# Performance work log

Measured on AMD Instinct MI355X. Metric: run time of the kernel, lower is better.

Reference implementation:

```python
import jax, jax.numpy as jnp
import numpy as np

N_NODES = 50000
N_EDGES = 800000
D_IN = 64
D_OUT = 64


def setup_inputs() -> dict:
    key = jax.random.key(0)
    k_feat, k_src, k_dst, k_ew, k_wn, k_bn, k_ws = jax.random.split(key, 7)
    feat = jax.random.normal(k_feat, (N_NODES, D_IN), dtype=jnp.float32)
    src = jax.random.randint(k_src, (N_EDGES,), 0, N_NODES, dtype=jnp.int64)
    dst = jax.random.randint(k_dst, (N_EDGES,), 0, N_NODES, dtype=jnp.int64)
    edge_weight = jax.random.uniform(k_ew, (N_EDGES,), dtype=jnp.float32)
    W_neigh = jax.random.normal(k_wn, (D_IN, D_OUT), dtype=jnp.float32) / np.sqrt(D_IN)
    b_neigh = jax.random.normal(k_bn, (D_OUT,), dtype=jnp.float32) * 0.01
    W_self = jax.random.normal(k_ws, (D_OUT, D_IN), dtype=jnp.float32) / np.sqrt(D_IN)
    return {"feat": feat, "src": src, "dst": dst, "edge_weight": edge_weight,
            "W_neigh": W_neigh, "b_neigh": b_neigh, "W_self": W_self}


def reference(feat, src, dst, edge_weight, W_neigh, b_neigh, W_self):
    # DGL GraphConv with norm='none': sum_{j in N(i)} e_ij * h_j, then @ W + b
    msg = feat[src] * edge_weight[:, None]                      # [E, D_in]
    agg = jax.ops.segment_sum(msg, dst, num_segments=feat.shape[0])  # [N, D_in]
    neigh_feat = agg @ W_neigh + b_neigh                        # [N, D_out]
    self_feat = feat @ W_self.T                                 # Linear, bias=False
    return neigh_feat + self_feat
```

## Files before the change

### kernel.cpp

```cpp
#include <hip/hip_runtime.h>

#define NN 50000
#define NE 800000
#define D 64
#define BN_SH 8
#define BNODES 256
#define NB 196
#define EPB 4096
#define NWB 196
#define CONV_B 800
#define BCAP 4608

constexpr size_t alignup(size_t x) { return (x + 1023) & ~size_t(1023); }
constexpr size_t OFF_EM   = 0;
constexpr size_t OFF_EM2  = alignup(OFF_EM + (size_t)NB * BCAP * 8);
constexpr size_t OFF_AGG  = alignup(OFF_EM2 + (size_t)NB * BCAP * 4);
constexpr size_t OFF_FB   = alignup(OFF_AGG + (size_t)NN * D * 4);
constexpr size_t OFF_RS2  = alignup(OFF_FB + (size_t)NN * D * 2);
constexpr size_t OFF_CUR  = alignup(OFF_RS2 + (size_t)NN * 8);

__device__ __forceinline__ unsigned f2bf(unsigned u) {
    return (u + 0x7FFFu + ((u >> 16) & 1u)) >> 16;
}

__global__ __launch_bounds__(256) void gc_zero(int* cur) {
    if (threadIdx.x < NB) cur[threadIdx.x] = 0;
}

__global__ __launch_bounds__(256) void bin_write(const int* __restrict__ src,
                                                 const int* __restrict__ dst,
                                                 const float* __restrict__ ew,
                                                 const float* __restrict__ feat,
                                                 int* __restrict__ cur,
                                                 uint2* __restrict__ em,
                                                 ushort* __restrict__ fb16) {
    int b = blockIdx.x;
    if (b >= NWB) {
        int cb = b - NWB;
        const float4* f4 = (const float4*)feat;
        ushort4* o4 = (ushort4*)fb16;
        for (int i = cb * 256 + threadIdx.x; i < NN * D / 4; i += CONV_B * 256) {
            float4 v = f4[i];
            ushort4 o;
            o.x = (ushort)f2bf(__float_as_uint(v.x));
            o.y = (ushort)f2bf(__float_as_uint(v.y));
            o.z = (ushort)f2bf(__float_as_uint(v.z));
            o.w = (ushort)f2bf(__float_as_uint(v.w));
            o4[i] = o;
        }
        return;
    }
    __shared__ int h[NB];
    __shared__ int gb[NB];
    for (int i = threadIdx.x; i < NB; i += 256) h[i] = 0;
    __syncthreads();
    int c0 = b * EPB;
    uint2 rec[16];
    int rk[16];
    int bk[16];
#pragma unroll
    for (int j = 0; j < 16; ++j) {
        int e = c0 + j * 256 + threadIdx.x;
        if (e < NE) {
            int dv = dst[e];
            int bb = dv >> BN_SH;
            bk[j] = bb;
            rk[j] = atomicAdd(&h[bb], 1);
            rec[j] = make_uint2((unsigned)src[e] | ((unsigned)(dv & (BNODES - 1)) << 16),
                                __float_as_uint(ew[e]));
        } else bk[j] = -1;
    }
    __syncthreads();
    for (int i = threadIdx.x; i < NB; i += 256) {
        int c = h[i];
        gb[i] = c ? atomicAdd(&cur[i], c) : 0;
    }
    __syncthreads();
#pragma unroll
    for (int j = 0; j < 16; ++j)
        if (bk[j] >= 0)
            em[(size_t)bk[j] * BCAP + gb[bk[j]] + rk[j]] = rec[j];
}

__global__ __launch_bounds__(256) void bucket_csr(const uint2* __restrict__ em,
                                                  const int* __restrict__ cur,
                                                  int2* __restrict__ rs2,
                                                  unsigned* __restrict__ em2) {
    __shared__ int hist[BNODES];
    __shared__ int lbase[BNODES];
    __shared__ int lcur[BNODES];
    __shared__ int sh[BNODES];
    int b = blockIdx.x;
    int t = threadIdx.x;
    int beg = b * BCAP;
    int end = beg + cur[b];
    hist[t] = 0;
    __syncthreads();
    for (int e = beg + t; e < end; e += 256)
        atomicAdd(&hist[(em[e].x >> 16) & 0xFFu], 1);
    __syncthreads();
    int v = hist[t];
    sh[t] = v;
    __syncthreads();
    for (int o = 1; o < 256; o <<= 1) {
        int x = (t >= o) ? sh[t - o] : 0;
        __syncthreads();
        sh[t] += x;
        __syncthreads();
    }
    int ex = sh[t] - v;
    lbase[t] = ex;
    lcur[t] = 0;
    int n = (b << BN_SH) + t;
    if (n < NN) rs2[n] = make_int2(beg + ex, beg + ex + v);
    __syncthreads();
    for (int e = beg + t; e < end; e += 256) {
        uint2 r = em[e];
        unsigned dl = (r.x >> 16) & 0xFFu;
        int pos = beg + lbase[dl] + atomicAdd(&lcur[dl], 1);
        em2[pos] = (r.x & 0xFFFFu) | (f2bf(r.y) << 16);
    }
}

__global__ __launch_bounds__(256) void gc_gather(const ushort* __restrict__ fb16,
                                                 const int2* __restrict__ rs2,
                                                 const unsigned* __restrict__ em2,
                                                 float* __restrict__ agg) {
    int wid = threadIdx.x >> 6;
    int lane = threadIdx.x & 63;
    int n = blockIdx.x * 4 + wid;
    if (n >= NN) return;
    int2 r2 = rs2[n];
    int beg = __builtin_amdgcn_readfirstlane(r2.x);
    int end = __builtin_amdgcn_readfirstlane(r2.y);
    float acc = 0.f;
    int e = beg;
    for (; e + 8 <= end; e += 8) {
        unsigned v[8];
#pragma unroll
        for (int j = 0; j < 8; ++j) v[j] = em2[e + j];
        float f[8];
#pragma unroll
        for (int j = 0; j < 8; ++j)
            f[j] = __uint_as_float((unsigned)fb16[(size_t)(v[j] & 0xFFFFu) * D + lane] << 16);
#pragma unroll
        for (int j = 0; j < 8; ++j)
            acc = fmaf(__uint_as_float(v[j] & 0xFFFF0000u), f[j], acc);
    }
    for (; e + 4 <= end; e += 4) {
        unsigned v0 = em2[e], v1 = em2[e + 1], v2 = em2[e + 2], v3 = em2[e + 3];
        float f0 = __uint_as_float((unsigned)fb16[(size_t)(v0 & 0xFFFFu) * D + lane] << 16);
        float f1 = __uint_as_float((unsigned)fb16[(size_t)(v1 & 0xFFFFu) * D + lane] << 16);
        float f2 = __uint_as_float((unsigned)fb16[(size_t)(v2 & 0xFFFFu) * D + lane] << 16);
        float f3 = __uint_as_float((unsigned)fb16[(size_t)(v3 & 0xFFFFu) * D + lane] << 16);
        acc = fmaf(__uint_as_float(v0 & 0xFFFF0000u), f0, acc);
        acc = fmaf(__uint_as_float(v1 & 0xFFFF0000u), f1, acc);
        acc = fmaf(__uint_as_float(v2 & 0xFFFF0000u), f2, acc);
        acc = fmaf(__uint_as_float(v3 & 0xFFFF0000u), f3, acc);
    }
    for (; e < end; ++e) {
        unsigned v = em2[e];
        float f = __uint_as_float((unsigned)fb16[(size_t)(v & 0xFFFFu) * D + lane] << 16);
        acc = fmaf(__uint_as_float(v & 0xFFFF0000u), f, acc);
    }
    agg[(size_t)n * D + lane] = acc;
}

#define BM 128
__global__ __launch_bounds__(256) void gemm_out(const float* __restrict__ agg,
                                                const float* __restrict__ feat,
                                                const float* __restrict__ Wn,
                                                const float* __restrict__ Ws,
                                                const float* __restrict__ bn,
                                                float* __restrict__ out) {
    __shared__ float Bs[128 * 64];
    __shared__ float As[BM * 36];
    int tid = threadIdx.x;
    for (int i = tid; i < 128 * 64; i += 256) {
        int k = i >> 6, d = i & 63;
        Bs[i] = (k < 64) ? Wn[i] : Ws[d * 64 + (k - 64)];
    }
    int tn = tid & 7;
    int tm = tid >> 3;
    float4 blo = *(const float4*)&bn[tn * 8];
    float4 bhi = *(const float4*)&bn[tn * 8 + 4];
    float acc[4][8];
#pragma unroll
    for (int i = 0; i < 4; ++i) {
        acc[i][0] = blo.x; acc[i][1] = blo.y; acc[i][2] = blo.z; acc[i][3] = blo.w;
        acc[i][4] = bhi.x; acc[i][5] = bhi.y; acc[i][6] = bhi.z; acc[i][7] = bhi.w;
    }
    int n0 = blockIdx.x * BM;
    for (int c = 0; c < 4; ++c) {
        const float* Asrc = (c < 2) ? agg : feat;
        int ksrc = (c & 1) * 32;
        __syncthreads();
        for (int i = tid; i < BM * 8; i += 256) {
            int r = i >> 3, c4 = i & 7;
            int nrow = n0 + r;
            const float* p = Asrc + (size_t)(nrow < NN ? nrow : 0) * 64 + ksrc + c4 * 4;
            float4 v = *(const float4*)p;
            float* q = &As[r * 36 + c4 * 4];
            q[0] = v.x; q[1] = v.y; q[2] = v.z; q[3] = v.w;
        }
        __syncthreads();
        int kb = c * 32;
#pragma unroll
        for (int k4 = 0; k4 < 8; ++k4) {
            float4 av[4];
#pragma unroll
            for (int i = 0; i < 4; ++i)
                av[i] = *(const float4*)&As[(tm + 32 * i) * 36 + k4 * 4];
#pragma unroll
            for (int kk = 0; kk < 4; ++kk) {
                int k = kb + k4 * 4 + kk;
                float4 wlo = *(const float4*)&Bs[k * 64 + tn * 8];
                float4 whi = *(const float4*)&Bs[k * 64 + tn * 8 + 4];
#pragma unroll
                for (int i = 0; i < 4; ++i) {
                    float a = (kk == 0) ? av[i].x : (kk == 1) ? av[i].y
                            : (kk == 2) ? av[i].z : av[i].w;
                    acc[i][0] = fmaf(a, wlo.x, acc[i][0]);
                    acc[i][1] = fmaf(a, wlo.y, acc[i][1]);
                    acc[i][2] = fmaf(a, wlo.z, acc[i][2]);
                    acc[i][3] = fmaf(a, wlo.w, acc[i][3]);
                    acc[i][4] = fmaf(a, whi.x, acc[i][4]);
                    acc[i][5] = fmaf(a, whi.y, acc[i][5]);
                    acc[i][6] = fmaf(a, whi.z, acc[i][6]);
                    acc[i][7] = fmaf(a, whi.w, acc[i][7]);
                }
            }
        }
    }
#pragma unroll
    for (int i = 0; i < 4; ++i) {
        int r = n0 + tm + 32 * i;
        if (r < NN) {
            float* p = &out[(size_t)r * 64 + tn * 8];
            *(float4*)p = make_float4(acc[i][0], acc[i][1], acc[i][2], acc[i][3]);
            *(float4*)(p + 4) = make_float4(acc[i][4], acc[i][5], acc[i][6], acc[i][7]);
        }
    }
}

extern "C" void kernel_launch(void* const* d_in, const int* in_sizes, int n_in,
                              void* d_out, int out_size, void* d_ws, size_t ws_size,
                              hipStream_t stream) {
    const float* feat = (const float*)d_in[0];
    const int*   src  = (const int*)d_in[1];
    const int*   dst  = (const int*)d_in[2];
    const float* ew   = (const float*)d_in[3];
    const float* Wn   = (const float*)d_in[4];
    const float* bn   = (const float*)d_in[5];
    const float* Ws   = (const float*)d_in[6];
    float* out = (float*)d_out;

    char* ws = (char*)d_ws;
    uint2*    em   = (uint2*)(ws + OFF_EM);
    unsigned* em2  = (unsigned*)(ws + OFF_EM2);
    float*    agg  = (float*)(ws + OFF_AGG);
    ushort*   fb16 = (ushort*)(ws + OFF_FB);
    int2*     rs2  = (int2*)(ws + OFF_RS2);
    int*      cur  = (int*)(ws + OFF_CUR);

    gc_zero<<<1, 256, 0, stream>>>(cur);
    bin_write<<<NWB + CONV_B, 256, 0, stream>>>(src, dst, ew, feat, cur, em, fb16);
    bucket_csr<<<NB, 256, 0, stream>>>(em, cur, rs2, em2);
    gc_gather<<<(NN + 3) / 4, 256, 0, stream>>>(fb16, rs2, em2, agg);
    gemm_out<<<(NN + BM - 1) / BM, 256, 0, stream>>>(agg, feat, Wn, Ws, bn, out);
}
```

Baseline: 84.50 us.

## Replace fp32 SIMT output GEMM with bf16 MFMA using bf16 aggregate and features

The gather kernel now writes the aggregated features as bf16 instead of fp32. The final dense projection is rewritten as a bf16 MFMA 16x16x32 GEMM that reads the bf16 aggregate and the existing bf16 feature copy, with the weights transposed and converted in LDS. This halves the intermediate traffic and moves the GEMM onto matrix cores. In exchange the self term and the aggregate both lose precision through bf16, and the output stores become scattered scalar writes.

Measured after the change: 71.23 us. 15.7% less time.

```diff
diff --git a/kernel.cpp b/kernel.cpp
--- a/kernel.cpp
+++ b/kernel.cpp
@@ -14,13 +14,19 @@
 constexpr size_t alignup(size_t x) { return (x + 1023) & ~size_t(1023); }
 constexpr size_t OFF_EM   = 0;
 constexpr size_t OFF_EM2  = alignup(OFF_EM + (size_t)NB * BCAP * 8);
-constexpr size_t OFF_AGG  = alignup(OFF_EM2 + (size_t)NB * BCAP * 4);
-constexpr size_t OFF_FB   = alignup(OFF_AGG + (size_t)NN * D * 4);
+constexpr size_t OFF_AGGB = alignup(OFF_EM2 + (size_t)NB * BCAP * 4);
+constexpr size_t OFF_FB   = alignup(OFF_AGGB + (size_t)NN * D * 2);
 constexpr size_t OFF_RS2  = alignup(OFF_FB + (size_t)NN * D * 2);
 constexpr size_t OFF_CUR  = alignup(OFF_RS2 + (size_t)NN * 8);
 
+typedef __attribute__((ext_vector_type(8))) short short8v;
+typedef __attribute__((ext_vector_type(4))) float float4v;
+
 __device__ __forceinline__ unsigned f2bf(unsigned u) {
     return (u + 0x7FFFu + ((u >> 16) & 1u)) >> 16;
+}
+__device__ __forceinline__ float bfu(unsigned short h) {
+    return __uint_as_float((unsigned)h << 16);
 }
 
 __global__ __launch_bounds__(256) void gc_zero(int* cur) {
@@ -125,7 +131,7 @@
 __global__ __launch_bounds__(256) void gc_gather(const ushort* __restrict__ fb16,
                                                  const int2* __restrict__ rs2,
                                                  const unsigned* __restrict__ em2,
-                                                 float* __restrict__ agg) {
+                                                 ushort* __restrict__ aggb) {
     int wid = threadIdx.x >> 6;
     int lane = threadIdx.x & 63;
     int n = blockIdx.x * 4 + wid;
@@ -142,17 +148,17 @@
         float f[8];
 #pragma unroll
         for (int j = 0; j < 8; ++j)
-            f[j] = __uint_as_float((unsigned)fb16[(size_t)(v[j] & 0xFFFFu) * D + lane] << 16);
+            f[j] = bfu(fb16[(size_t)(v[j] & 0xFFFFu) * D + lane]);
 #pragma unroll
         for (int j = 0; j < 8; ++j)
             acc = fmaf(__uint_as_float(v[j] & 0xFFFF0000u), f[j], acc);
     }
     for (; e + 4 <= end; e += 4) {
         unsigned v0 = em2[e], v1 = em2[e + 1], v2 = em2[e + 2], v3 = em2[e + 3];
-        float f0 = __uint_as_float((unsigned)fb16[(size_t)(v0 & 0xFFFFu) * D + lane] << 16);
-        float f1 = __uint_as_float((unsigned)fb16[(size_t)(v1 & 0xFFFFu) * D + lane] << 16);
-        float f2 = __uint_as_float((unsigned)fb16[(size_t)(v2 & 0xFFFFu) * D + lane] << 16);
-        float f3 = __uint_as_float((unsigned)fb16[(size_t)(v3 & 0xFFFFu) * D + lane] << 16);
+        float f0 = bfu(fb16[(size_t)(v0 & 0xFFFFu) * D + lane]);
+        float f1 = bfu(fb16[(size_t)(v1 & 0xFFFFu) * D + lane]);
+        float f2 = bfu(fb16[(size_t)(v2 & 0xFFFFu) * D + lane]);
+        float f3 = bfu(fb16[(size_t)(v3 & 0xFFFFu) * D + lane]);
         acc = fmaf(__uint_as_float(v0 & 0xFFFF0000u), f0, acc);
         acc = fmaf(__uint_as_float(v1 & 0xFFFF0000u), f1, acc);
         acc = fmaf(__uint_as_float(v2 & 0xFFFF0000u), f2, acc);
@@ -160,85 +166,64 @@
     }
     for (; e < end; ++e) {
         unsigned v = em2[e];
-        float f = __uint_as_float((unsigned)fb16[(size_t)(v & 0xFFFFu) * D + lane] << 16);
+        float f = bfu(fb16[(size_t)(v & 0xFFFFu) * D + lane]);
         acc = fmaf(__uint_as_float(v & 0xFFFF0000u), f, acc);
     }
-    agg[(size_t)n * D + lane] = acc;
-}
-
-#define BM 128
-__global__ __launch_bounds__(256) void gemm_out(const float* __restrict__ agg,
-                                                const float* __restrict__ feat,
-                                                const float* __restrict__ Wn,
-                                                const float* __restrict__ Ws,
-                                                const float* __restrict__ bn,
-                                                float* __restrict__ out) {
-    __shared__ float Bs[128 * 64];
-    __shared__ float As[BM * 36];
+    aggb[(size_t)n * D + lane] = (ushort)f2bf(__float_as_uint(acc));
+}
+
+__global__ __launch_bounds__(256) void gemm_mfma(const ushort* __restrict__ aggb,
+                                                 const ushort* __restrict__ fb16,
+                                                 const float* __restrict__ Wn,
+                                                 const float* __restrict__ Ws,
+                                                 const float* __restrict__ bn,
+                                                 float* __restrict__ out) {
+    __shared__ ushort Bt[64 * 136];
     int tid = threadIdx.x;
-    for (int i = tid; i < 128 * 64; i += 256) {
-        int k = i >> 6, d = i & 63;
-        Bs[i] = (k < 64) ? Wn[i] : Ws[d * 64 + (k - 64)];
-    }
-    int tn = tid & 7;
-    int tm = tid >> 3;
-    float4 blo = *(const float4*)&bn[tn * 8];
-    float4 bhi = *(const float4*)&bn[tn * 8 + 4];
-    float acc[4][8];
-#pragma unroll
-    for (int i = 0; i < 4; ++i) {
-        acc[i][0] = blo.x; acc[i][1] = blo.y; acc[i][2] = blo.z; acc[i][3] = blo.w;
-        acc[i][4] = bhi.x; acc[i][5] = bhi.y; acc[i][6] = bhi.z; acc[i][7] = bhi.w;
-    }
-    int n0 = blockIdx.x * BM;
+    for (int i = tid; i < 64 * 128; i += 256) {
+        int col = i & 63, k = i >> 6;
+        float v = (k < 64) ? Wn[k * 64 + col] : Ws[col * 64 + (k - 64)];
+        Bt[col * 136 + k] = (ushort)f2bf(__float_as_uint(v));
+    }
+    __syncthreads();
+    int w = tid >> 6, lane = tid & 63;
+    int lr = lane & 15;
+    int lk = lane >> 4;
+    int n0 = blockIdx.x * 128 + w * 32;
+    float4v acc[2][4];
+#pragma unroll
     for (int c = 0; c < 4; ++c) {
-        const float* Asrc = (c < 2) ? agg : feat;
-        int ksrc = (c & 1) * 32;
-        __syncthreads();
-        for (int i = tid; i < BM * 8; i += 256) {
-            int r = i >> 3, c4 = i & 7;
-            int nrow = n0 + r;
-            const float* p = Asrc + (size_t)(nrow < NN ? nrow : 0) * 64 + ksrc + c4 * 4;
-            float4 v = *(const float4*)p;
-            float* q = &As[r * 36 + c4 * 4];
-            q[0] = v.x; q[1] = v.y; q[2] = v.z; q[3] = v.w;
+        float bv = bn[c * 16 + lr];
+        acc[0][c] = (float4v){bv, bv, bv, bv};
+        acc[1][c] = (float4v){bv, bv, bv, bv};
+    }
+    int r0 = min(n0 + lr, NN - 1);
+    int r1 = min(n0 + 16 + lr, NN - 1);
+#pragma unroll
+    for (int kc = 0; kc < 4; ++kc) {
+        const ushort* At = (kc < 2) ? aggb : fb16;
+        int bk = (kc & 1) * 32 + lk * 8;
+        short8v a0 = *(const short8v*)(At + (size_t)r0 * 64 + bk);
+        short8v a1 = *(const short8v*)(At + (size_t)r1 * 64 + bk);
+        int kg = kc * 32 + lk * 8;
+#pragma unroll
+        for (int c = 0; c < 4; ++c) {
+            short8v bf = *(const short8v*)(&Bt[(c * 16 + lr) * 136 + kg]);
+            acc[0][c] = __builtin_amdgcn_mfma_f32_16x16x32_bf16(a0, bf, acc[0][c], 0, 0, 0);
+            acc[1][c] = __builtin_amdgcn_mfma_f32_16x16x32_bf16(a1, bf, acc[1][c], 0, 0, 0);
         }
-        __syncthreads();
-        int kb = c * 32;
-#pragma unroll
-        for (int k4 = 0; k4 < 8; ++k4) {
-            float4 av[4];
-#pragma unroll
-            for (int i = 0; i < 4; ++i)
-                av[i] = *(const float4*)&As[(tm + 32 * i) * 36 + k4 * 4];
-#pragma unroll
-            for (int kk = 0; kk < 4; ++kk) {
-                int k = kb + k4 * 4 + kk;
-                float4 wlo = *(const float4*)&Bs[k * 64 + tn * 8];
-                float4 whi = *(const float4*)&Bs[k * 64 + tn * 8 + 4];
-#pragma unroll
-                for (int i = 0; i < 4; ++i) {
-                    float a = (kk == 0) ? av[i].x : (kk == 1) ? av[i].y
-                            : (kk == 2) ? av[i].z : av[i].w;
-                    acc[i][0] = fmaf(a, wlo.x, acc[i][0]);
-                    acc[i][1] = fmaf(a, wlo.y, acc[i][1]);
-                    acc[i][2] = fmaf(a, wlo.z, acc[i][2]);
-                    acc[i][3] = fmaf(a, wlo.w, acc[i][3]);
-                    acc[i][4] = fmaf(a, whi.x, acc[i][4]);
-                    acc[i][5] = fmaf(a, whi.y, acc[i][5]);
-                    acc[i][6] = fmaf(a, whi.z, acc[i][6]);
-                    acc[i][7] = fmaf(a, whi.w, acc[i][7]);
-                }
+    }
+#pragma unroll
+    for (int r = 0; r < 2; ++r) {
+        int rowb = n0 + r * 16 + lk * 4;
+#pragma unroll
+        for (int c = 0; c < 4; ++c) {
+            int col = c * 16 + lr;
+#pragma unroll
+            for (int j = 0; j < 4; ++j) {
+                int row = rowb + j;
+                if (row < NN) out[(size_t)row * 64 + col] = acc[r][c][j];
             }
-        }
-    }
-#pragma unroll
-    for (int i = 0; i < 4; ++i) {
-        int r = n0 + tm + 32 * i;
-        if (r < NN) {
-            float* p = &out[(size_t)r * 64 + tn * 8];
-            *(float4*)p = make_float4(acc[i][0], acc[i][1], acc[i][2], acc[i][3]);
-            *(float4*)(p + 4) = make_float4(acc[i][4], acc[i][5], acc[i][6], acc[i][7]);
         }
     }
 }
@@ -258,7 +243,7 @@
     char* ws = (char*)d_ws;
     uint2*    em   = (uint2*)(ws + OFF_EM);
     unsigned* em2  = (unsigned*)(ws + OFF_EM2);
-    float*    agg  = (float*)(ws + OFF_AGG);
+    ushort*   aggb = (ushort*)(ws + OFF_AGGB);
     ushort*   fb16 = (ushort*)(ws + OFF_FB);
     int2*     rs2  = (int2*)(ws + OFF_RS2);
     int*      cur  = (int*)(ws + OFF_CUR);
@@ -266,6 +251,6 @@
     gc_zero<<<1, 256, 0, stream>>>(cur);
     bin_write<<<NWB + CONV_B, 256, 0, stream>>>(src, dst, ew, feat, cur, em, fb16);
     bucket_csr<<<NB, 256, 0, stream>>>(em, cur, rs2, em2);
-    gc_gather<<<(NN + 3) / 4, 256, 0, stream>>>(fb16, rs2, em2, agg);
-    gemm_out<<<(NN + BM - 1) / BM, 256, 0, stream>>>(agg, feat, Wn, Ws, bn, out);
-}
+    gc_gather<<<(NN + 3) / 4, 256, 0, stream>>>(fb16, rs2, em2, aggb);
+    gemm_mfma<<<(NN + 127) / 128, 256, 0, stream>>>(aggb, fb16, Wn, Ws, bn, out);
+}
```
